# Performance work log

Measured on AMD Instinct MI355X. Metric: run time of the kernel, lower is better.

The kernel has to match this reference:

```python
import jax, jax.numpy as jnp
import numpy as np

_CLIP_MIN = 1e-6
_POS_ALPHA = 1e-3
RADIUS = 3
HALF_D = RADIUS * RADIUS  # 9: patch vector length per class
N_FINE, N_MID, N_HIGH = 19, 7, 3
LAMBDA = 0.5
LOSS_WEIGHT = 1.0
IGNORE = 255

_F2M = np.array([0,0,0,1,1,1,2,2,3,3,4,5,5,6,6,6,6,6,6], dtype=np.int64)
_M2H = np.array([0,0,1,1,1,2,2], dtype=np.int64)
_F2H = _M2H[_F2M]


def setup_inputs():
    key = jax.random.key(0)
    k1, k2, k3, k4 = jax.random.split(key, 4)
    B, H, W, D = 4, 512, 512, 256
    return {
        "step": 5000,
        "embedding": jax.random.normal(k1, (B, D, H // 8, W // 8), jnp.float32),
        "cls_score_before": jax.random.normal(k2, (B, N_FINE, H // 8, W // 8), jnp.float32),
        "cls_score": jax.random.normal(k3, (B, N_FINE + N_MID + N_HIGH, H, W), jnp.float32),
        "label": jax.random.randint(k4, (B, H, W), 0, N_FINE),
        "fine_to_mid": jnp.asarray(_F2M),
        "fine_to_high": jnp.asarray(_F2H),
    }


def _maxpool3(x):  # kernel=stride=3, VALID (rmi_pool_way=0)
    return jax.lax.reduce_window(x, -jnp.inf, jax.lax.max, (1, 1, 3, 3), (1, 1, 3, 3), "VALID")


def _map_get_pairs(la, pr, radius=RADIUS):
    b, c, h, w = la.shape
    nh, nw = h - radius + 1, w - radius + 1
    las = [la[:, :, y:y + nh, x:x + nw] for y in range(radius) for x in range(radius)]
    prs = [pr[:, :, y:y + nh, x:x + nw] for y in range(radius) for x in range(radius)]
    la_v = jnp.stack(las, axis=2).reshape(b, c, radius * radius, nh * nw)
    pr_v = jnp.stack(prs, axis=2).reshape(b, c, radius * radius, nh * nw)
    return la_v, pr_v


def _rmi_lower_bound(oh, probs, vmask):
    # oh, probs: [B,C,H,W]; vmask: [B,1,H,W]
    la = _maxpool3(oh * vmask)
    pr = _maxpool3(probs * vmask + _CLIP_MIN)
    la_v, pr_v = _map_get_pairs(la, pr)  # [B,C,half_d,N]
    la_v = jax.lax.stop_gradient(la_v)   # labels are detached in the original
    la_v = la_v - la_v.mean(axis=-1, keepdims=True)
    pr_v = pr_v - pr_v.mean(axis=-1, keepdims=True)
    diag = _POS_ALPHA * jnp.eye(HALF_D, dtype=la_v.dtype)
    pr_cov = jnp.einsum("bcdn,bcen->bcde", pr_v, pr_v) + diag
    la_cov = jnp.einsum("bcdn,bcen->bcde", la_v, la_v)
    la_pr = jnp.einsum("bcdn,bcen->bcde", la_v, pr_v)
    appro = la_cov - la_pr @ jnp.linalg.solve(pr_cov, jnp.swapaxes(la_pr, -1, -2)) + diag
    chol = jnp.linalg.cholesky(appro)
    logdet = 2.0 * jnp.sum(jnp.log(jnp.diagonal(chol, axis1=-2, axis2=-1) + 1e-8), axis=-1)  # [B,C]
    return jnp.sum(logdet.mean(axis=0) / HALF_D)


def _hiera_bce(oh, pos, neg, vmask):
    # positives judged against min-combined probs, negatives against max-combined probs
    loss = -(oh * jnp.log(pos + 1e-8) + (1.0 - oh) * jnp.log(1.0 - neg + 1e-8)) * vmask
    return loss.sum() / (vmask.sum() * oh.shape[1] + 1e-8)


def _forward(cls_score, label, fine_to_mid, fine_to_high):
    probs = jax.nn.sigmoid(cls_score.astype(jnp.float32))
    valid = (label != IGNORE)
    vmask = valid[:, None].astype(jnp.float32)  # [B,1,H,W]
    lf = jnp.where(valid, label, 0)
    lm = fine_to_mid[lf]
    lh = fine_to_high[lf]
    oh_f = jax.nn.one_hot(lf, N_FINE, axis=1, dtype=jnp.float32)
    oh_m = jax.nn.one_hot(lm, N_MID, axis=1, dtype=jnp.float32)
    oh_h = jax.nn.one_hot(lh, N_HIGH, axis=1, dtype=jnp.float32)
    MCMA = probs[:, :N_FINE]
    MCMB = probs[:, N_FINE:N_FINE + N_MID]
    MCMC = probs[:, N_FINE + N_MID:]
    # upward (max) hierarchy consistency
    segf = jax.ops.segment_max(jnp.moveaxis(MCMA, 1, 0), fine_to_mid, num_segments=N_MID)
    MCMB_c = jnp.maximum(jnp.moveaxis(segf, 0, 1), MCMB)
    mid_to_high = jnp.zeros((N_MID,), dtype=fine_to_high.dtype).at[fine_to_mid].set(fine_to_high)
    segm = jax.ops.segment_max(jnp.moveaxis(MCMB_c, 1, 0), mid_to_high, num_segments=N_HIGH)
    MCMC_c = jnp.maximum(jnp.moveaxis(segm, 0, 1), MCMC)
    # downward (min) hierarchy consistency
    MCLA = jnp.minimum(MCMA, MCMB[:, fine_to_mid])
    MCLB_c = jnp.minimum(MCMB, MCMC[:, mid_to_high])
    MCLC_c = MCMC
    total = 0.0
    for oh, pos, neg in ((oh_f, MCLA, MCMA), (oh_m, MCLB_c, MCMB_c), (oh_h, MCLC_c, MCMC_c)):
        bce = _hiera_bce(oh, pos, neg, vmask)
        rmi = _rmi_lower_bound(oh, pos, vmask)
        total = total + LAMBDA * bce + (1.0 - LAMBDA) * rmi
    return LOSS_WEIGHT * total


def reference(step, embedding, cls_score_before, cls_score, label, fine_to_mid, fine_to_high):
    # step / embedding / cls_score_before feed only the triplet branch (not in provided source)
    return _forward(cls_score, label, fine_to_mid, fine_to_high)
```

## Files before the change

### kernel.cpp

```cpp
#include <hip/hip_runtime.h>
#include <math.h>

namespace {
constexpr int NB = 4, NCHT = 29, NF = 19, NM = 7, NHI = 3;
constexpr int HH = 512, WW = 512;
constexpr int PH  = 170;
constexpr int NHW = 168;
constexpr int NS  = NHW * NHW;
constexpr int NBC = NB * NCHT;
constexpr int CROWS = 14;
constexpr int NCH2  = NHW / CROWS;

constexpr int F2M[NF] = {0,0,0,1,1,1,2,2,3,3,4,5,5,6,6,6,6,6,6};
constexpr int M2H[NM] = {0,0,1,1,1,2,2};
constexpr int F2H[NF] = {0,0,0,0,0,0,1,1,1,1,1,2,2,2,2,2,2,2,2};

constexpr unsigned long long packTbl(const int* a, int n) {
  unsigned long long p = 0;
  for (int i = 0; i < n; i++) p |= (unsigned long long)(a[i]) << (3 * i);
  return p;
}
constexpr unsigned long long PF2M = packTbl(F2M, NF);
constexpr unsigned long long PF2H = packTbl(F2H, NF);

constexpr int    WS_S1  = 16;
constexpr int    WS_COV = 4096;
constexpr int    WS_RED = 49152;
constexpr size_t WS_LA  = 65536;
constexpr size_t WS_PR  = WS_LA + (size_t)NBC * PH * PH;
constexpr size_t WS_ZERO_BYTES = (size_t)(WS_RED + 64 * 16) * 4;
}

__global__ __launch_bounds__(128, 2)
void kA(const float* __restrict__ cls, const int* __restrict__ label,
        float* __restrict__ ws) {
  const int bx  = blockIdx.x;
  const int wy  = blockIdx.y;
  const int b   = blockIdx.z;
  const int tid = threadIdx.x;

  __shared__ float    sPr[102][30];
  __shared__ unsigned sMask[102];
  __shared__ float    sRed[4][2];

  float bce0 = 0.f, bce1 = 0.f, bce2 = 0.f, cnt = 0.f;

  const bool pool   = (tid < 102);
  const bool hasCol = pool || (bx == 4 && tid < 104);
  const bool row2   = (wy < 170);

  if (hasCol) {
    const int x  = 102 * bx + tid;
    const int y0 = 3 * wy;
    const size_t lpix = ((size_t)b * HH + y0) * WW + x;
    const int off2 = row2 ? 2 * WW : 0;
    const int l0 = label[lpix];
    const int l1 = label[lpix + WW];
    const int l2 = label[lpix + off2];

    const float* cp = cls + ((size_t)(b * NCHT) * HH + y0) * WW + x;
    float r0v[NCHT], r1v[NCHT], r2v[NCHT];
    #pragma unroll
    for (int c = 0; c < NCHT; c++) r0v[c] = cp[(size_t)c * HH * WW];
    #pragma unroll
    for (int c = 0; c < NCHT; c++) r1v[c] = cp[(size_t)c * HH * WW + WW];
    #pragma unroll
    for (int c = 0; c < NCHT; c++) r2v[c] = cp[(size_t)c * HH * WW + off2];

    float colPr[NCHT];
    #pragma unroll
    for (int c = 0; c < NCHT; c++) colPr[c] = 0.f;
    unsigned msk = 0u;

    auto doRow = [&](const float* rv, int lbl, bool act) {
      const bool valid = act && (lbl != 255);
      const int lf = valid ? lbl : 0;
      const int lm = (int)((PF2M >> (3 * lf)) & 7ull);
      const int lh = (int)((PF2H >> (3 * lf)) & 7ull);
      const float vm = valid ? 1.f : 0.f;

      float p[NCHT];
      #pragma unroll
      for (int c = 0; c < NCHT; c++)
        p[c] = __builtin_amdgcn_rcpf(1.f + __expf(-rv[c]));

      float segf[NM];
      #pragma unroll
      for (int m = 0; m < NM; m++) segf[m] = -1.f;
      #pragma unroll
      for (int f = 0; f < NF; f++) segf[F2M[f]] = fmaxf(segf[F2M[f]], p[f]);
      float pBc[NM];
      #pragma unroll
      for (int m = 0; m < NM; m++) pBc[m] = fmaxf(segf[m], p[NF + m]);
      float segm[NHI];
      #pragma unroll
      for (int k = 0; k < NHI; k++) segm[k] = -1.f;
      #pragma unroll
      for (int m = 0; m < NM; m++) segm[M2H[m]] = fmaxf(segm[M2H[m]], pBc[m]);
      float pCc[NHI];
      #pragma unroll
      for (int k = 0; k < NHI; k++) pCc[k] = fmaxf(segm[k], p[NF + NM + k]);

      #pragma unroll
      for (int f = 0; f < NF; f++) {
        const float pos = fminf(p[f], p[NF + F2M[f]]);
        if (valid)
          bce0 += (f == lf) ? -__logf(pos + 1e-8f) : -__logf(1.f - p[f] + 1e-8f);
        colPr[f] = fmaxf(colPr[f], pos * vm + 1e-6f);
      }
      #pragma unroll
      for (int m = 0; m < NM; m++) {
        const float pos = fminf(p[NF + m], p[NF + NM + M2H[m]]);
        if (valid)
          bce1 += (m == lm) ? -__logf(pos + 1e-8f) : -__logf(1.f - pBc[m] + 1e-8f);
        colPr[NF + m] = fmaxf(colPr[NF + m], pos * vm + 1e-6f);
      }
      #pragma unroll
      for (int k = 0; k < NHI; k++) {
        const float pos = p[NF + NM + k];
        if (valid)
          bce2 += (k == lh) ? -__logf(pos + 1e-8f) : -__logf(1.f - pCc[k] + 1e-8f);
        colPr[NF + NM + k] = fmaxf(colPr[NF + NM + k], pos * vm + 1e-6f);
      }
      if (valid) {
        msk |= 1u << lf;
        msk |= 1u << (19 + lm);
        msk |= 1u << (26 + lh);
      }
      cnt += vm;
    };

    doRow(r0v, l0, true);
    doRow(r1v, l1, true);
    doRow(r2v, l2, row2);

    if (pool) {
      sMask[tid] = msk;
      #pragma unroll
      for (int c = 0; c < NCHT; c++) sPr[tid][c] = colPr[c];
    }
  }

  #pragma unroll
  for (int m = 32; m >= 1; m >>= 1) {
    bce0 += __shfl_xor(bce0, m);
    bce1 += __shfl_xor(bce1, m);
    bce2 += __shfl_xor(bce2, m);
    cnt  += __shfl_xor(cnt, m);
  }
  {
    const int wave = tid >> 6, lane = tid & 63;
    if (lane == 0) {
      sRed[0][wave] = bce0; sRed[1][wave] = bce1;
      sRed[2][wave] = bce2; sRed[3][wave] = cnt;
    }
  }
  __syncthreads();

  if (row2 && tid < 34) {
    const int wx = 34 * bx + tid;
    const int c0 = 3 * tid;
    float* la = ws + WS_LA;
    float* pr = ws + WS_PR;
    const unsigned m = sMask[c0] | sMask[c0 + 1] | sMask[c0 + 2];
    const size_t base = ((size_t)(b * NCHT) * PH + wy) * PH + wx;
    #pragma unroll
    for (int c = 0; c < NF; c++)
      la[base + (size_t)c * PH * PH] = (float)((m >> c) & 1u);
    #pragma unroll
    for (int mm = 0; mm < NM; mm++)
      la[base + (size_t)(NF + mm) * PH * PH] = (float)((m >> (19 + mm)) & 1u);
    #pragma unroll
    for (int k = 0; k < NHI; k++)
      la[base + (size_t)(NF + NM + k) * PH * PH] = (float)((m >> (26 + k)) & 1u);
    #pragma unroll
    for (int c = 0; c < NCHT; c++)
      pr[base + (size_t)c * PH * PH] =
          fmaxf(fmaxf(sPr[c0][c], sPr[c0 + 1][c]), sPr[c0 + 2][c]);
  }

  if (tid == 0) {
    const int slot = (bx + 5 * (wy + 171 * b)) & 63;
    float* dst = ws + WS_RED + slot * 16;
    atomicAdd(&dst[0], sRed[0][0] + sRed[0][1]);
    atomicAdd(&dst[1], sRed[1][0] + sRed[1][1]);
    atomicAdd(&dst[2], sRed[2][0] + sRed[2][1]);
    atomicAdd(&dst[3], sRed[3][0] + sRed[3][1]);
  }
}

__global__ __launch_bounds__(192)
void kCov(const float* __restrict__ ws_base, float* __restrict__ cov,
          float* __restrict__ s1out) {
  const int bc    = blockIdx.x / NCH2;
  const int chunk = blockIdx.x % NCH2;
  const int tid   = threadIdx.x;
  const int tile  = tid / 32;
  const int g     = tid % 32;
  const int ta = (tile < 3) ? 0 : ((tile < 5) ? 1 : 2);
  const int tb = (tile < 3) ? tile : ((tile < 5) ? tile - 2 : 2);
  const bool diag = (ta == tb);

  __shared__ float sA[16 * PH];
  __shared__ float sP[16 * PH];

  const int r0 = chunk * CROWS;
  const float* Ag = ws_base + WS_LA + (size_t)bc * PH * PH + (size_t)r0 * PH;
  const float* Pg = ws_base + WS_PR + (size_t)bc * PH * PH + (size_t)r0 * PH;
  for (int i = tid; i < 16 * PH; i += 192) { sA[i] = Ag[i]; sP[i] = Pg[i]; }
  __syncthreads();

  const float* baseA[6];
  const float* baseB[6];
  #pragma unroll
  for (int k = 0; k < 6; k++) {
    int r = 6 * ta + k, rr = r % 9;
    baseA[k] = ((r < 9) ? sA : sP) + (rr / 3) * PH + (rr % 3);
    int r2 = 6 * tb + k, rr2 = r2 % 9;
    baseB[k] = ((r2 < 9) ? sA : sP) + (rr2 / 3) * PH + (rr2 % 3);
  }

  float acc[6][6];
  #pragma unroll
  for (int k = 0; k < 6; k++)
    #pragma unroll
    for (int l = 0; l < 6; l++) acc[k][l] = 0.f;
  float sums[6];
  #pragma unroll
  for (int k = 0; k < 6; k++) sums[k] = 0.f;

  for (int lr = 0; lr < CROWS; lr++) {
    const int rowoff = lr * PH;
    for (int lc = g; lc < NHW; lc += 32) {
      float va[6], vb[6];
      #pragma unroll
      for (int k = 0; k < 6; k++) va[k] = baseA[k][rowoff + lc];
      #pragma unroll
      for (int k = 0; k < 6; k++) vb[k] = baseB[k][rowoff + lc];
      #pragma unroll
      for (int k = 0; k < 6; k++)
        #pragma unroll
        for (int l = 0; l < 6; l++) acc[k][l] = fmaf(va[k], vb[l], acc[k][l]);
      if (diag) {
        #pragma unroll
        for (int k = 0; k < 6; k++) sums[k] += va[k];
      }
    }
  }

  #pragma unroll
  for (int k = 0; k < 6; k++)
    #pragma unroll
    for (int l = 0; l < 6; l++) {
      float v = acc[k][l];
      #pragma unroll
      for (int m = 16; m >= 1; m >>= 1) v += __shfl_xor(v, m);
      acc[k][l] = v;
    }
  if (diag) {
    #pragma unroll
    for (int k = 0; k < 6; k++) {
      float v = sums[k];
      #pragma unroll
      for (int m = 16; m >= 1; m >>= 1) v += __shfl_xor(v, m);
      sums[k] = v;
    }
  }
  if (g == 0) {
    float* dst = cov + (size_t)bc * 324;
    #pragma unroll
    for (int k = 0; k < 6; k++)
      #pragma unroll
      for (int l = 0; l < 6; l++)
        atomicAdd(&dst[(6 * ta + k) * 18 + 6 * tb + l], acc[k][l]);
    if (diag) {
      #pragma unroll
      for (int k = 0; k < 6; k++)
        atomicAdd(&s1out[bc * 32 + 6 * ta + k], sums[k]);
    }
  }
}

__global__ __launch_bounds__(64)
void kSolve(const float* __restrict__ cov_all, const float* __restrict__ s1,
            float* __restrict__ acc) {
  const int bc   = blockIdx.x;
  const int lane = threadIdx.x;
  const float* cr = cov_all + (size_t)bc * 324;
  const double n = (double)NS;

  double mu[18];
  #pragma unroll
  for (int r = 0; r < 18; r++) mu[r] = (double)s1[bc * 32 + r] / n;
#define CC(i, j) ((double)cr[(i) * 18 + (j)] - n * mu[(i)] * mu[(j)])

  double row[9];
  #pragma unroll
  for (int j = 0; j < 9; j++)
    row[j] = (lane < 9 && j <= lane) ? CC(9 + j, 9 + lane) : 0.0;
  if (lane < 9) row[lane] += 1e-3;

  #pragma unroll
  for (int k = 0; k < 9; k++) {
    if (lane == k) {
      double s = row[k];
      #pragma unroll
      for (int m = 0; m < k; m++) s -= row[m] * row[m];
      row[k] = sqrt(fmax(s, 1e-300));
    }
    double rk[9];
    #pragma unroll
    for (int m = 0; m <= k; m++) rk[m] = __shfl(row[m], k);
    if (lane > k && lane < 9) {
      double s = row[k];
      #pragma unroll
      for (int m = 0; m < k; m++) s -= row[m] * rk[m];
      row[k] = s / rk[k];
    }
  }

  double Lm[9][9];
  #pragma unroll
  for (int i = 0; i < 9; i++)
    #pragma unroll
    for (int m = 0; m <= i; m++) Lm[i][m] = __shfl(row[m], i);

  double mc[9];
  #pragma unroll
  for (int r = 0; r < 9; r++) mc[r] = 0.0;
  if (lane < 9) {
    #pragma unroll
    for (int r = 0; r < 9; r++) {
      double s = CC(lane, 9 + r);
      #pragma unroll
      for (int m = 0; m < r; m++) s -= Lm[r][m] * mc[m];
      mc[r] = s / Lm[r][r];
    }
  }

  double a2[9];
  #pragma unroll
  for (int j = 0; j < 9; j++) a2[j] = 0.0;
  #pragma unroll
  for (int j = 0; j < 9; j++) {
    double mj[9];
    #pragma unroll
    for (int r = 0; r < 9; r++) mj[r] = __shfl(mc[r], j);
    double dot = 0.0;
    #pragma unroll
    for (int r = 0; r < 9; r++) dot += mc[r] * mj[r];
    if (lane < 9 && j <= lane)
      a2[j] = CC(j, lane) - dot + ((j == lane) ? 1e-3 : 0.0);
  }
#undef CC

  double myld = 0.0;
  #pragma unroll
  for (int k = 0; k < 9; k++) {
    if (lane == k) {
      double s = a2[k];
      #pragma unroll
      for (int m = 0; m < k; m++) s -= a2[m] * a2[m];
      double d = sqrt(fmax(s, 0.0));
      a2[k] = d;
      myld = 2.0 * log(d + 1e-8);
    }
    double rk[9];
    #pragma unroll
    for (int m = 0; m <= k; m++) rk[m] = __shfl(a2[m], k);
    if (lane > k && lane < 9) {
      double s = a2[k];
      #pragma unroll
      for (int m = 0; m < k; m++) s -= a2[m] * rk[m];
      a2[k] = s / rk[k];
    }
  }
  #pragma unroll
  for (int m = 32; m >= 1; m >>= 1) myld += __shfl_xor(myld, m);
  if (lane == 0) atomicAdd(&acc[4], (float)myld);
}

__global__ void kFin(const float* __restrict__ ws, float* __restrict__ out) {
  const int tid = threadIdx.x;
  const float* slot = ws + WS_RED + tid * 16;
  float b0 = slot[0], b1 = slot[1], b2 = slot[2], b3 = slot[3];
  #pragma unroll
  for (int m = 32; m >= 1; m >>= 1) {
    b0 += __shfl_xor(b0, m);
    b1 += __shfl_xor(b1, m);
    b2 += __shfl_xor(b2, m);
    b3 += __shfl_xor(b3, m);
  }
  if (tid == 0) {
    const double cnt = (double)b3;
    const double bce = 0.5 * ((double)b0 / (cnt * NF + 1e-8) +
                              (double)b1 / (cnt * NM + 1e-8) +
                              (double)b2 / (cnt * NHI + 1e-8));
    const double rmi = 0.5 * (double)ws[4] / (double)(NB * 9);
    out[0] = (float)(bce + rmi);
  }
}

extern "C" void kernel_launch(void* const* d_in, const int* in_sizes, int n_in,
                              void* d_out, int out_size, void* d_ws, size_t ws_size,
                              hipStream_t stream) {
  (void)in_sizes; (void)n_in; (void)out_size; (void)ws_size;
  const float* cls   = (const float*)d_in[3];
  const int*   label = (const int*)d_in[4];
  float* ws = (float*)d_ws;

  hipMemsetAsync(d_ws, 0, WS_ZERO_BYTES, stream);

  dim3 gA(5, 171, NB);
  kA<<<gA, 128, 0, stream>>>(cls, label, ws);
  kCov<<<NBC * NCH2, 192, 0, stream>>>(ws, ws + WS_COV, ws + WS_S1);
  kSolve<<<NBC, 64, 0, stream>>>(ws + WS_COV, ws + WS_S1, ws);
  kFin<<<1, 64, 0, stream>>>(ws, (float*)d_out);
}
```

Baseline: 132.2 us.

## Restructure kA to one pixel per thread with shared-memory staging

kA now stages the 3x104x29 input tile into shared memory cooperatively, then gives each of 256 threads one pixel instead of one column of three rows. Per-pixel probabilities and masks are written back into shared memory, and the 3x3 max-pool is done in the write-out phase. This is meant to cut register pressure (the old version held 87 floats per thread) and raise occupancy and memory-level parallelism. In exchange it adds a barrier and more LDS traffic, and 312 pixels over 256 threads leaves most threads idle in a second pass.

```diff
diff --git a/kernel.cpp b/kernel.cpp
--- a/kernel.cpp
+++ b/kernel.cpp
@@ -31,67 +31,60 @@
 constexpr size_t WS_ZERO_BYTES = (size_t)(WS_RED + 64 * 16) * 4;
 }
 
-__global__ __launch_bounds__(128, 2)
+__global__ __launch_bounds__(256, 4)
 void kA(const float* __restrict__ cls, const int* __restrict__ label,
         float* __restrict__ ws) {
   const int bx  = blockIdx.x;
   const int wy  = blockIdx.y;
   const int b   = blockIdx.z;
   const int tid = threadIdx.x;
-
-  __shared__ float    sPr[102][30];
-  __shared__ unsigned sMask[102];
-  __shared__ float    sRed[4][2];
+  const int x0  = 102 * bx;
+  const int y0  = 3 * wy;
+
+  __shared__ float    sPix[NCHT][312];
+  __shared__ unsigned sMask[312];
+  __shared__ float    sRed[4][4];
+
+  const int rmax = (wy == 170) ? 1 : 2;
+
+  for (int i = tid; i < NCHT * 312; i += 256) {
+    const int c   = i / 312;
+    const int rem = i - c * 312;
+    const int r   = rem / 104;
+    const int x   = rem - r * 104;
+    const int rr  = (r <= rmax) ? r : rmax;
+    sPix[c][rem] = cls[((size_t)(b * NCHT + c) * HH + (y0 + rr)) * WW + x0 + x];
+  }
+  __syncthreads();
 
   float bce0 = 0.f, bce1 = 0.f, bce2 = 0.f, cnt = 0.f;
-
-  const bool pool   = (tid < 102);
-  const bool hasCol = pool || (bx == 4 && tid < 104);
-  const bool row2   = (wy < 170);
-
-  if (hasCol) {
-    const int x  = 102 * bx + tid;
-    const int y0 = 3 * wy;
-    const size_t lpix = ((size_t)b * HH + y0) * WW + x;
-    const int off2 = row2 ? 2 * WW : 0;
-    const int l0 = label[lpix];
-    const int l1 = label[lpix + WW];
-    const int l2 = label[lpix + off2];
-
-    const float* cp = cls + ((size_t)(b * NCHT) * HH + y0) * WW + x;
-    float r0v[NCHT], r1v[NCHT], r2v[NCHT];
-    #pragma unroll
-    for (int c = 0; c < NCHT; c++) r0v[c] = cp[(size_t)c * HH * WW];
-    #pragma unroll
-    for (int c = 0; c < NCHT; c++) r1v[c] = cp[(size_t)c * HH * WW + WW];
-    #pragma unroll
-    for (int c = 0; c < NCHT; c++) r2v[c] = cp[(size_t)c * HH * WW + off2];
-
-    float colPr[NCHT];
-    #pragma unroll
-    for (int c = 0; c < NCHT; c++) colPr[c] = 0.f;
-    unsigned msk = 0u;
-
-    auto doRow = [&](const float* rv, int lbl, bool act) {
-      const bool valid = act && (lbl != 255);
+  for (int p = tid; p < 312; p += 256) {
+    const int r   = p / 104;
+    const int col = p - r * 104;
+    const bool realRow = (r <= rmax);
+    const bool owned   = (col < 102) || (bx == 4);
+    if (realRow && owned) {
+      const int y = y0 + r, x = x0 + col;
+      const int lbl = label[((size_t)b * HH + y) * WW + x];
+      const bool valid = (lbl != 255);
       const int lf = valid ? lbl : 0;
       const int lm = (int)((PF2M >> (3 * lf)) & 7ull);
       const int lh = (int)((PF2H >> (3 * lf)) & 7ull);
       const float vm = valid ? 1.f : 0.f;
 
-      float p[NCHT];
+      float pv[NCHT];
       #pragma unroll
       for (int c = 0; c < NCHT; c++)
-        p[c] = __builtin_amdgcn_rcpf(1.f + __expf(-rv[c]));
+        pv[c] = __builtin_amdgcn_rcpf(1.f + __expf(-sPix[c][p]));
 
       float segf[NM];
       #pragma unroll
       for (int m = 0; m < NM; m++) segf[m] = -1.f;
       #pragma unroll
-      for (int f = 0; f < NF; f++) segf[F2M[f]] = fmaxf(segf[F2M[f]], p[f]);
+      for (int f = 0; f < NF; f++) segf[F2M[f]] = fmaxf(segf[F2M[f]], pv[f]);
       float pBc[NM];
       #pragma unroll
-      for (int m = 0; m < NM; m++) pBc[m] = fmaxf(segf[m], p[NF + m]);
+      for (int m = 0; m < NM; m++) pBc[m] = fmaxf(segf[m], pv[NF + m]);
       float segm[NHI];
       #pragma unroll
       for (int k = 0; k < NHI; k++) segm[k] = -1.f;
@@ -99,45 +92,39 @@
       for (int m = 0; m < NM; m++) segm[M2H[m]] = fmaxf(segm[M2H[m]], pBc[m]);
       float pCc[NHI];
       #pragma unroll
-      for (int k = 0; k < NHI; k++) pCc[k] = fmaxf(segm[k], p[NF + NM + k]);
+      for (int k = 0; k < NHI; k++) pCc[k] = fmaxf(segm[k], pv[NF + NM + k]);
 
       #pragma unroll
       for (int f = 0; f < NF; f++) {
-        const float pos = fminf(p[f], p[NF + F2M[f]]);
+        const float pos = fminf(pv[f], pv[NF + F2M[f]]);
         if (valid)
-          bce0 += (f == lf) ? -__logf(pos + 1e-8f) : -__logf(1.f - p[f] + 1e-8f);
-        colPr[f] = fmaxf(colPr[f], pos * vm + 1e-6f);
+          bce0 += (f == lf) ? -__logf(pos + 1e-8f) : -__logf(1.f - pv[f] + 1e-8f);
+        sPix[f][p] = pos * vm + 1e-6f;
       }
       #pragma unroll
       for (int m = 0; m < NM; m++) {
-        const float pos = fminf(p[NF + m], p[NF + NM + M2H[m]]);
+        const float pos = fminf(pv[NF + m], pv[NF + NM + M2H[m]]);
         if (valid)
           bce1 += (m == lm) ? -__logf(pos + 1e-8f) : -__logf(1.f - pBc[m] + 1e-8f);
-        colPr[NF + m] = fmaxf(colPr[NF + m], pos * vm + 1e-6f);
+        sPix[NF + m][p] = pos * vm + 1e-6f;
       }
       #pragma unroll
       for (int k = 0; k < NHI; k++) {
-        const float pos = p[NF + NM + k];
+        const float pos = pv[NF + NM + k];
         if (valid)
           bce2 += (k == lh) ? -__logf(pos + 1e-8f) : -__logf(1.f - pCc[k] + 1e-8f);
-        colPr[NF + NM + k] = fmaxf(colPr[NF + NM + k], pos * vm + 1e-6f);
+        sPix[NF + NM + k][p] = pos * vm + 1e-6f;
       }
+      unsigned msk = 0u;
       if (valid) {
-        msk |= 1u << lf;
-        msk |= 1u << (19 + lm);
-        msk |= 1u << (26 + lh);
+        msk = (1u << lf) | (1u << (19 + lm)) | (1u << (26 + lh));
       }
+      sMask[p] = msk;
       cnt += vm;
-    };
-
-    doRow(r0v, l0, true);
-    doRow(r1v, l1, true);
-    doRow(r2v, l2, row2);
-
-    if (pool) {
-      sMask[tid] = msk;
-      #pragma unroll
-      for (int c = 0; c < NCHT; c++) sPr[tid][c] = colPr[c];
+    } else if (owned) {
+      #pragma unroll
+      for (int c = 0; c < NCHT; c++) sPix[c][p] = 0.f;
+      sMask[p] = 0u;
     }
   }
 
@@ -157,12 +144,15 @@
   }
   __syncthreads();
 
-  if (row2 && tid < 34) {
+  if (wy < 170 && tid < 34) {
     const int wx = 34 * bx + tid;
     const int c0 = 3 * tid;
     float* la = ws + WS_LA;
     float* pr = ws + WS_PR;
-    const unsigned m = sMask[c0] | sMask[c0 + 1] | sMask[c0 + 2];
+    unsigned m = 0u;
+    #pragma unroll
+    for (int r = 0; r < 3; r++)
+      m |= sMask[r * 104 + c0] | sMask[r * 104 + c0 + 1] | sMask[r * 104 + c0 + 2];
     const size_t base = ((size_t)(b * NCHT) * PH + wy) * PH + wx;
     #pragma unroll
     for (int c = 0; c < NF; c++)
@@ -174,18 +164,23 @@
     for (int k = 0; k < NHI; k++)
       la[base + (size_t)(NF + NM + k) * PH * PH] = (float)((m >> (26 + k)) & 1u);
     #pragma unroll
-    for (int c = 0; c < NCHT; c++)
-      pr[base + (size_t)c * PH * PH] =
-          fmaxf(fmaxf(sPr[c0][c], sPr[c0 + 1][c]), sPr[c0 + 2][c]);
+    for (int c = 0; c < NCHT; c++) {
+      float v = 0.f;
+      #pragma unroll
+      for (int r = 0; r < 3; r++)
+        v = fmaxf(v, fmaxf(fmaxf(sPix[c][r * 104 + c0], sPix[c][r * 104 + c0 + 1]),
+                           sPix[c][r * 104 + c0 + 2]));
+      pr[base + (size_t)c * PH * PH] = v;
+    }
   }
 
   if (tid == 0) {
     const int slot = (bx + 5 * (wy + 171 * b)) & 63;
     float* dst = ws + WS_RED + slot * 16;
-    atomicAdd(&dst[0], sRed[0][0] + sRed[0][1]);
-    atomicAdd(&dst[1], sRed[1][0] + sRed[1][1]);
-    atomicAdd(&dst[2], sRed[2][0] + sRed[2][1]);
-    atomicAdd(&dst[3], sRed[3][0] + sRed[3][1]);
+    atomicAdd(&dst[0], sRed[0][0] + sRed[0][1] + sRed[0][2] + sRed[0][3]);
+    atomicAdd(&dst[1], sRed[1][0] + sRed[1][1] + sRed[1][2] + sRed[1][3]);
+    atomicAdd(&dst[2], sRed[2][0] + sRed[2][1] + sRed[2][2] + sRed[2][3]);
+    atomicAdd(&dst[3], sRed[3][0] + sRed[3][1] + sRed[3][2] + sRed[3][3]);
   }
 }
 
@@ -412,7 +407,7 @@
   hipMemsetAsync(d_ws, 0, WS_ZERO_BYTES, stream);
 
   dim3 gA(5, 171, NB);
-  kA<<<gA, 128, 0, stream>>>(cls, label, ws);
+  kA<<<gA, 256, 0, stream>>>(cls, label, ws);
   kCov<<<NBC * NCH2, 192, 0, stream>>>(ws, ws + WS_COV, ws + WS_S1);
   kSolve<<<NBC, 64, 0, stream>>>(ws + WS_COV, ws + WS_S1, ws);
   kFin<<<1, 64, 0, stream>>>(ws, (float*)d_out);
```

Measured after the change: 150.7 us. 1.14x slower.
